# Optimization experiments

Measured on AMD Instinct MI355X. Metric: run time of the kernel, lower is better.

Reference implementation:

```python
import jax, jax.numpy as jnp
import numpy as np

N = 100_000; E = 1_600_000; H = 64
TH = 0.7; ATT_TH = 0.2; EPS = 1e-5

# Heaviside spike with ATan surrogate gradient (spikingjelly default style).
@jax.custom_vjp
def spike_fn(v):
    return (v >= 0.0).astype(v.dtype)

def _spike_fwd(v):
    return spike_fn(v), v

def _spike_bwd(v, g):
    alpha = 2.0
    sg = (alpha / 2.0) / (1.0 + (jnp.pi / 2.0 * alpha * v) ** 2)
    return (g * sg,)

spike_fn.defvjp(_spike_fwd, _spike_bwd)

def lif_step(v, x, th):
    # integrate-and-fire step with hard reset-to-zero
    v = v + x
    s = spike_fn(v - th)
    return s, v * (1.0 - s)

def batchnorm(x, g, b):
    # training-mode BatchNorm1d over the node axis
    m = x.mean(axis=0)
    var = x.var(axis=0)
    return (x - m) * jax.lax.rsqrt(var + EPS) * g + b

def gcn(x, W, b, src, dst, w):
    # PyG GCNConv: xW, add self loops, symmetric deg^-1/2 normalization, scatter-add
    xw = x @ W                                   # [N,H]
    deg = jnp.ones((x.shape[0],), x.dtype).at[dst].add(w)   # self-loop weight 1
    dis = jax.lax.rsqrt(deg)
    norm = dis[src] * w * dis[dst]               # [E]
    agg = jnp.zeros_like(xw).at[dst].add(norm[:, None] * xw[src])
    return agg + (dis * dis)[:, None] * xw + b   # self-loop term + bias

def enc(x, src, dst, w, Wg, bg, bn_g, bn_b, v_conv):
    # Wg order: convs[0], conv, pos_conv, q_lins, k_lins, v_lins, att_conv
    # bn order:  bn_1, bn_2, pos_bn, pos_bn_2, q_bn, k_bn, v_bn, att_bn, att_bn_2
    x = batchnorm(gcn(x, Wg[0], bg[0], src, dst, w), bn_g[0], bn_b[0])
    x, v_conv = lif_step(v_conv, x, TH)          # conv_lif (stateful, never reset)
    x = batchnorm(gcn(x, Wg[1], bg[1], src, dst, w), bn_g[1], bn_b[1])
    z = jnp.zeros_like(x)
    # SGPE positional branch (pos_lif is reset after enc -> fresh state)
    x_pos_spike, _ = lif_step(z, x, TH)
    x_pos = batchnorm(gcn(x_pos_spike, Wg[2], bg[2], src, dst, w), bn_g[2], bn_b[2])
    x = batchnorm(x_pos + x, bn_g[3], bn_b[3])
    # attention branch: conv_lif second (stateful) call
    x_att, v_conv = lif_step(v_conv, x, TH)
    q, _ = lif_step(z, batchnorm(gcn(x_att, Wg[3], bg[3], src, dst, w), bn_g[4], bn_b[4]), TH)
    k, _ = lif_step(z, batchnorm(gcn(x_att, Wg[4], bg[4], src, dst, w), bn_g[5], bn_b[5]), TH)
    v, _ = lif_step(z, batchnorm(gcn(x_att, Wg[5], bg[5], src, dst, w), bn_g[6], bn_b[6]), TH)
    qk = (q * k).mean(axis=1)                    # [N]  (num_attention_heads == 1 path)
    qk, _ = lif_step(jnp.zeros_like(qk), qk, ATT_TH)
    att = qk[:, None] * v                        # repeat(H,1).T * v
    att = batchnorm(gcn(att, Wg[6], bg[6], src, dst, w), bn_g[7], bn_b[7])
    x = batchnorm(x + 0.125 * att, bn_g[8], bn_b[8])
    return x, v_conv

def setup_inputs():
    key = jax.random.key(0)
    ks = jax.random.split(key, 6)
    x = jax.random.normal(ks[0], (N, H), jnp.float32)
    edge_index = jax.random.randint(ks[1], (2, E), 0, N)
    edge_mask = jax.random.randint(ks[2], (E,), 0, 2, jnp.int32)
    Wg = jax.random.normal(ks[3], (7, H, H), jnp.float32) / jnp.sqrt(H)
    bg = jnp.zeros((7, H), jnp.float32)
    bn_g = jnp.ones((9, H), jnp.float32)
    bn_b = jnp.zeros((9, H), jnp.float32)
    W_lin = jax.random.normal(ks[4], (H, H), jnp.float32) / jnp.sqrt(H)
    return {"x": x, "edge_index": edge_index, "edge_mask": edge_mask,
            "Wg": Wg, "bg": bg, "bn_g": bn_g, "bn_b": bn_b, "W_lin": W_lin}

def reference(x, edge_index, edge_mask, Wg, bg, bn_g, bn_b, W_lin):
    src, dst = edge_index[0], edge_index[1]
    w1 = jnp.ones((E,), x.dtype)
    w2 = edge_mask.astype(x.dtype)   # dropout_edge(p=0.2) realized as fixed mask (weight 0 == removed edge)
    v0 = jnp.zeros((N, H), x.dtype)
    s1, v_conv = enc(x, src, dst, w1, Wg, bg, bn_g, bn_b, v0)
    s2, _ = enc(x, src, dst, w2, Wg, bg, bn_g, bn_b, v_conv)  # conv_lif state carries over
    z1 = (s1 @ W_lin).sum(axis=1)    # dec: lin(x).sum(1)
    z2 = (s2 @ W_lin).sum(axis=1)
    return (z1, z2)
```

## Files before the change

### kernel.cpp

```cpp
#include <hip/hip_runtime.h>
#include <math.h>
#include <stdint.h>
#include <limits.h>

#define NN 100000
#define NE 1600000
#define HH 64
#define THF 0.7f
#define ATTTH 0.2f
#define EPSF 1e-5f
#define SCAN_B ((NN + 255) / 256)
#define EM2CAP 1000000
#define NBE 2048
#define NHTOT ((size_t)NN * 64)
#define NB_ROW4C (NN / 4)
#define NTILE (NN / 32)

typedef unsigned long long u64;


__global__ void hist_k(const int* __restrict__ dst, const int* __restrict__ mask,
                       int* __restrict__ cnt_all, int* __restrict__ cnt_mask) {
    int e = blockIdx.x * 256 + threadIdx.x;
    if (e >= NE) return;
    int d = dst[e];
    atomicAdd(&cnt_all[d], 1);
    if (mask[e]) atomicAdd(&cnt_mask[d], 1);
}

__global__ void deg_inv2_k(const int* __restrict__ cnt1, const int* __restrict__ cnt2,
                           float* __restrict__ dis1, float* __restrict__ d21,
                           float* __restrict__ dis2m, float* __restrict__ d22) {
    int i = blockIdx.x * 256 + threadIdx.x;
    if (i < NN) {
        float dg1 = (float)(cnt1[i] + 1);
        dis1[i] = 1.0f / sqrtf(dg1);
        d21[i] = 1.0f / dg1;
        float dg2 = (float)(cnt2[i] + 1);
        dis2m[i] = 1.0f / sqrtf(dg2);
        d22[i] = 1.0f / dg2;
    }
}

__global__ void scan1d_k(const int* __restrict__ cnt1, const int* __restrict__ cnt2,
                         int* __restrict__ rp1, int* __restrict__ rp2,
                         int* __restrict__ bsum) {
    __shared__ int ls[256];
    int half = (blockIdx.x >= SCAN_B) ? 1 : 0;
    int blk = blockIdx.x - half * SCAN_B;
    const int* counts = half ? cnt2 : cnt1;
    int* rp = half ? rp2 : rp1;
    int i = blk * 256 + threadIdx.x;
    int v = (i < NN) ? counts[i] : 0;
    ls[threadIdx.x] = v;
    __syncthreads();
    for (int off = 1; off < 256; off <<= 1) {
        int t = (threadIdx.x >= off) ? ls[threadIdx.x - off] : 0;
        __syncthreads();
        ls[threadIdx.x] += t;
        __syncthreads();
    }
    if (i < NN) rp[i] = ls[threadIdx.x] - v;
    if (threadIdx.x == 255) bsum[blockIdx.x] = ls[255];
}

__global__ __launch_bounds__(512) void scan2d_k(int* __restrict__ bsum,
                                                int* __restrict__ rp1,
                                                int* __restrict__ rp2) {
    __shared__ int ls[512];
    int i = threadIdx.x;
    for (int s = 0; s < 2; s++) {
        int v = (i < SCAN_B) ? bsum[s * SCAN_B + i] : 0;
        ls[i] = v;
        __syncthreads();
        for (int off = 1; off < 512; off <<= 1) {
            int t = (i >= off) ? ls[i - off] : 0;
            __syncthreads();
            ls[i] += t;
            __syncthreads();
        }
        if (i < SCAN_B) bsum[s * SCAN_B + i] = ls[i] - v;
        if (i == SCAN_B - 1) { if (s == 0) rp1[NN] = ls[i]; else rp2[NN] = ls[i]; }
        __syncthreads();
    }
}

__global__ void scan3d_k(int* __restrict__ rp1, int* __restrict__ rp2,
                         const int* __restrict__ bsum) {
    int half = (blockIdx.x >= SCAN_B) ? 1 : 0;
    int blk = blockIdx.x - half * SCAN_B;
    int* rp = half ? rp2 : rp1;
    int i = blk * 256 + threadIdx.x;
    if (i < NN) rp[i] += bsum[blockIdx.x];
}

__global__ void csr_fill_k(const int* __restrict__ src, const int* __restrict__ dst,
                           const int* __restrict__ mask,
                           const int* __restrict__ rp1, const int* __restrict__ rp2,
                           int* __restrict__ cur1, int* __restrict__ cur2,
                           int* __restrict__ emA, int* __restrict__ emB) {
    int e = blockIdx.x * 256 + threadIdx.x;
    if (e >= NE) return;
    int s = src[e], d = dst[e];
    int mk = mask[e] & 1;
    int p1 = rp1[d] + atomicAdd(&cur1[d], 1);
    emA[p1] = (s << 1) | mk;
    if (mk) {
        int p2 = rp2[d] + atomicAdd(&cur2[d], 1);
        emB[p2] = s;
    }
}

__device__ void seg_sort_node(int* __restrict__ em, int beg, int end,
                              int* skey, int lane) {
    int L = end - beg;
    if (L <= 1) return;
    if (L <= 64) {
        int k = (lane < L) ? em[beg + lane] : INT_MAX;
        int rank = 0;
#pragma unroll 8
        for (int r = 0; r < L; r++) {
            int kr = __shfl(k, r, 64);
            rank += (kr < k || (kr == k && r < lane)) ? 1 : 0;
        }
        if (lane < L) em[beg + rank] = k;
    } else if (L <= 512) {
        for (int i = lane; i < L; i += 64) skey[i] = em[beg + i];
        for (int it = 0; it < L; it++) {
            int par = it & 1;
            for (int p = par + 2 * lane; p + 1 < L; p += 128) {
                int ka = skey[p], kb = skey[p + 1];
                if (kb < ka) { skey[p] = kb; skey[p + 1] = ka; }
            }
        }
        for (int i = lane; i < L; i += 64) em[beg + i] = skey[i];
    }
}

__global__ __launch_bounds__(256) void seg_sort2_k(int* __restrict__ emA,
                                                   const int* __restrict__ rp1,
                                                   int* __restrict__ emB,
                                                   const int* __restrict__ rp2) {
    __shared__ int skey[4][512];
    int tid = threadIdx.x, lane = tid & 63, w = tid >> 6;
    int bid = blockIdx.x;
    if (bid < NB_ROW4C) {
        int n = bid * 4 + w;
        seg_sort_node(emA, rp1[n], rp1[n + 1], skey[w], lane);
    } else {
        int n = (bid - NB_ROW4C) * 4 + w;
        seg_sort_node(emB, rp2[n], rp2[n + 1], skey[w], lane);
    }
}


__global__ __launch_bounds__(256) void gemm_k(const float* __restrict__ in,
                                              const float* __restrict__ W,
                                              float* __restrict__ xw) {
    __shared__ float sW[64 * 64];
    __shared__ float sx[32 * 65];
    int tid = threadIdx.x;
    const float4* W4 = (const float4*)W;
    float4* sW4 = (float4*)sW;
    for (int i = tid; i < 1024; i += 256) sW4[i] = W4[i];
    const float* inb = in + (size_t)blockIdx.x * 2048;
    for (int i = tid; i < 2048; i += 256) sx[(i >> 6) * 65 + (i & 63)] = inb[i];
    __syncthreads();
    int cg = tid & 15, rr = tid >> 4;
    float a0 = 0, a1 = 0, a2 = 0, a3 = 0, c0 = 0, c1 = 0, c2 = 0, c3 = 0;
#pragma unroll
    for (int k = 0; k < 64; k++) {
        float4 wv = *(const float4*)&sW[k * 64 + cg * 4];
        float xa = sx[rr * 65 + k];
        float xb = sx[(rr + 16) * 65 + k];
        a0 += xa * wv.x; a1 += xa * wv.y; a2 += xa * wv.z; a3 += xa * wv.w;
        c0 += xb * wv.x; c1 += xb * wv.y; c2 += xb * wv.z; c3 += xb * wv.w;
    }
    size_t r0 = (size_t)(blockIdx.x * 32 + rr) * 64 + cg * 4;
    size_t r1 = (size_t)(blockIdx.x * 32 + rr + 16) * 64 + cg * 4;
    *(float4*)&xw[r0] = make_float4(a0, a1, a2, a3);
    *(float4*)&xw[r1] = make_float4(c0, c1, c2, c3);
}


__global__ __launch_bounds__(256) void gather_stats_k(const float* __restrict__ xw,
                                                      const int* __restrict__ em,
                                                      int shift,
                                                      const float* __restrict__ dis,
                                                      const int* __restrict__ rp,
                                                      const float* __restrict__ d2i,
                                                      const float* __restrict__ bias,
                                                      float* __restrict__ out,
                                                      double* __restrict__ part) {
    int tid = threadIdx.x, lane = tid & 63, w = tid >> 6;
    double ps = 0.0, pq = 0.0;
    for (int n = blockIdx.x * 4 + w; n < NN; n += NBE * 4) {
        int beg = rp[n], end = rp[n + 1];
        float disn = dis[n];
        float self = d2i[n] * xw[(size_t)n * 64 + lane] + bias[lane];
        float acc = 0.0f;
        for (int base = beg; base < end; base += 64) {
            int cnt = min(64, end - base);
            int m = 0; float nl = 0.0f;
            if (base + lane < end) {
                m = em[base + lane];
                nl = dis[m >> shift] * disn;
            }
            int j = 0;
            for (; j + 8 <= cnt; j += 8) {
#pragma unroll
                for (int u = 0; u < 8; u++) {
                    int s = __shfl(m, j + u, 64) >> shift;
                    float nv = __shfl(nl, j + u, 64);
                    acc += nv * xw[(size_t)s * 64 + lane];
                }
            }
            for (; j < cnt; j++) {
                int s = __shfl(m, j, 64) >> shift;
                float nv = __shfl(nl, j, 64);
                acc += nv * xw[(size_t)s * 64 + lane];
            }
        }
        float o = acc + self;
        out[(size_t)n * 64 + lane] = o;
        ps += (double)o;
        pq += (double)o * (double)o;
    }
    __shared__ double ls[4][64], lq[4][64];
    ls[w][lane] = ps; lq[w][lane] = pq;
    __syncthreads();
    if (tid < 64) {
        double a = ls[0][tid] + ls[1][tid] + ls[2][tid] + ls[3][tid];
        double b = lq[0][tid] + lq[1][tid] + lq[2][tid] + lq[3][tid];
        part[(size_t)blockIdx.x * 128 + tid] = a;
        part[(size_t)blockIdx.x * 128 + 64 + tid] = b;
    }
}

__global__ __launch_bounds__(256) void sharedL0_k(const float* __restrict__ xw,
                                                  const int* __restrict__ em,
                                                  const int* __restrict__ rp,
                                                  const float* __restrict__ dis1,
                                                  const float* __restrict__ dis2m,
                                                  const float* __restrict__ d21,
                                                  const float* __restrict__ d22,
                                                  const float* __restrict__ bias,
                                                  float* __restrict__ o1,
                                                  float* __restrict__ o2,
                                                  double* __restrict__ part) {
    int tid = threadIdx.x, lane = tid & 63, w = tid >> 6;
    double sA = 0.0, qA = 0.0, sB = 0.0, qB = 0.0;
    for (int n = blockIdx.x * 4 + w; n < NN; n += NBE * 4) {
        int beg = rp[n], end = rp[n + 1];
        float disn1 = dis1[n], disn2 = dis2m[n];
        float xv = xw[(size_t)n * 64 + lane];
        float self1 = d21[n] * xv + bias[lane];
        float self2 = d22[n] * xv + bias[lane];
        float acc1 = 0.0f, acc2 = 0.0f;
        for (int base = beg; base < end; base += 64) {
            int cnt = min(64, end - base);
            int m = 0; float nl1 = 0.0f, nl2 = 0.0f;
            if (base + lane < end) {
                m = em[base + lane];
                int s = m >> 1;
                nl1 = dis1[s] * disn1;
                nl2 = dis2m[s] * disn2;
            }
            int j = 0;
            for (; j + 8 <= cnt; j += 8) {
#pragma unroll
                for (int u = 0; u < 8; u++) {
                    int key = __shfl(m, j + u, 64);
                    int s = key >> 1;
                    float n1 = __shfl(nl1, j + u, 64);
                    float n2 = __shfl(nl2, j + u, 64);
                    float v = xw[(size_t)s * 64 + lane];
                    acc1 += n1 * v;
                    acc2 += (key & 1) ? n2 * v : 0.0f;
                }
            }
            for (; j < cnt; j++) {
                int key = __shfl(m, j, 64);
                int s = key >> 1;
                float n1 = __shfl(nl1, j, 64);
                float n2 = __shfl(nl2, j, 64);
                float v = xw[(size_t)s * 64 + lane];
                acc1 += n1 * v;
                acc2 += (key & 1) ? n2 * v : 0.0f;
            }
        }
        size_t o = (size_t)n * 64 + lane;
        float v1 = acc1 + self1;
        float v2 = acc2 + self2;
        o1[o] = v1;
        o2[o] = v2;
        sA += (double)v1; qA += (double)v1 * (double)v1;
        sB += (double)v2; qB += (double)v2 * (double)v2;
    }
    __shared__ double l1[4][64], l2[4][64], l3[4][64], l4[4][64];
    l1[w][lane] = sA; l2[w][lane] = qA; l3[w][lane] = sB; l4[w][lane] = qB;
    __syncthreads();
    if (tid < 64) {
        size_t o = (size_t)blockIdx.x * 256;
        part[o + tid]       = l1[0][tid] + l1[1][tid] + l1[2][tid] + l1[3][tid];
        part[o + 64 + tid]  = l2[0][tid] + l2[1][tid] + l2[2][tid] + l2[3][tid];
        part[o + 128 + tid] = l3[0][tid] + l3[1][tid] + l3[2][tid] + l3[3][tid];
        part[o + 192 + tid] = l4[0][tid] + l4[1][tid] + l4[2][tid] + l4[3][tid];
    }
}


__global__ __launch_bounds__(256) void bitagg_k(const u64* __restrict__ bits,
                                                const int* __restrict__ em,
                                                int shift,
                                                const float* __restrict__ dis,
                                                const int* __restrict__ rp,
                                                const float* __restrict__ d2i,
                                                float* __restrict__ A) {
    int tid = threadIdx.x, lane = tid & 63, w = tid >> 6;
    int sh31 = lane & 31;
    bool islo = lane < 32;
    for (int n = blockIdx.x * 4 + w; n < NN; n += NBE * 4) {
        int beg = rp[n], end = rp[n + 1];
        float disn = dis[n];
        float acc = 0.0f;
        for (int base = beg; base < end; base += 64) {
            int cnt = min(64, end - base);
            unsigned blo = 0, bhi = 0; float nl = 0.0f;
            if (base + lane < end) {
                int m = em[base + lane];
                int s = m >> shift;
                nl = dis[s] * disn;
                u64 b = bits[s];
                blo = (unsigned)b;
                bhi = (unsigned)(b >> 32);
            }
            int j = 0;
            for (; j + 8 <= cnt; j += 8) {
#pragma unroll
                for (int u = 0; u < 8; u++) {
                    float nv = __shfl(nl, j + u, 64);
                    unsigned lo = (unsigned)__shfl((int)blo, j + u, 64);
                    unsigned hi = (unsigned)__shfl((int)bhi, j + u, 64);
                    unsigned sel = islo ? lo : hi;
                    acc += ((sel >> sh31) & 1u) ? nv : 0.0f;
                }
            }
            for (; j < cnt; j++) {
                float nv = __shfl(nl, j, 64);
                unsigned lo = (unsigned)__shfl((int)blo, j, 64);
                unsigned hi = (unsigned)__shfl((int)bhi, j, 64);
                unsigned sel = islo ? lo : hi;
                acc += ((sel >> sh31) & 1u) ? nv : 0.0f;
            }
        }
        u64 bn = bits[n];
        unsigned seln = islo ? (unsigned)bn : (unsigned)(bn >> 32);
        acc += ((seln >> sh31) & 1u) ? d2i[n] : 0.0f;
        A[(size_t)n * 64 + lane] = acc;
    }
}


__global__ __launch_bounds__(256) void gemmb_stats_k(const float* __restrict__ A,
                                                     const float* __restrict__ W,
                                                     const float* __restrict__ bias,
                                                     float* __restrict__ G,
                                                     double* __restrict__ part,
                                                     int pstride, int pbase) {
    __shared__ float sW[64 * 64];
    __shared__ float sx[32 * 65];
    __shared__ double sS[64][16], sQ[64][16];
    int tid = threadIdx.x;
    const float4* W4 = (const float4*)W;
    float4* sW4 = (float4*)sW;
    for (int i = tid; i < 1024; i += 256) sW4[i] = W4[i];
    int cg = tid & 15, rr = tid >> 4;
    float4 bv = *(const float4*)&bias[cg * 4];
    double s0 = 0, s1 = 0, s2 = 0, s3 = 0, q0 = 0, q1 = 0, q2 = 0, q3 = 0;
    for (int tile = blockIdx.x; tile < NTILE; tile += NBE) {
        const float* Ab = A + (size_t)tile * 2048;
        __syncthreads();
        for (int i = tid; i < 2048; i += 256) sx[(i >> 6) * 65 + (i & 63)] = Ab[i];
        __syncthreads();
        float a0 = bv.x, a1 = bv.y, a2 = bv.z, a3 = bv.w;
        float c0 = bv.x, c1 = bv.y, c2 = bv.z, c3 = bv.w;
#pragma unroll
        for (int k = 0; k < 64; k++) {
            float4 wv = *(const float4*)&sW[k * 64 + cg * 4];
            float xa = sx[rr * 65 + k];
            float xb = sx[(rr + 16) * 65 + k];
            a0 += xa * wv.x; a1 += xa * wv.y; a2 += xa * wv.z; a3 += xa * wv.w;
            c0 += xb * wv.x; c1 += xb * wv.y; c2 += xb * wv.z; c3 += xb * wv.w;
        }
        size_t r0 = (size_t)(tile * 32 + rr) * 64 + cg * 4;
        size_t r1 = (size_t)(tile * 32 + rr + 16) * 64 + cg * 4;
        *(float4*)&G[r0] = make_float4(a0, a1, a2, a3);
        *(float4*)&G[r1] = make_float4(c0, c1, c2, c3);
        s0 += (double)a0; s0 += (double)c0;
        s1 += (double)a1; s1 += (double)c1;
        s2 += (double)a2; s2 += (double)c2;
        s3 += (double)a3; s3 += (double)c3;
        q0 += (double)a0 * (double)a0; q0 += (double)c0 * (double)c0;
        q1 += (double)a1 * (double)a1; q1 += (double)c1 * (double)c1;
        q2 += (double)a2 * (double)a2; q2 += (double)c2 * (double)c2;
        q3 += (double)a3 * (double)a3; q3 += (double)c3 * (double)c3;
    }
    __syncthreads();
    sS[cg * 4 + 0][rr] = s0; sQ[cg * 4 + 0][rr] = q0;
    sS[cg * 4 + 1][rr] = s1; sQ[cg * 4 + 1][rr] = q1;
    sS[cg * 4 + 2][rr] = s2; sQ[cg * 4 + 2][rr] = q2;
    sS[cg * 4 + 3][rr] = s3; sQ[cg * 4 + 3][rr] = q3;
    __syncthreads();
    if (tid < 64) {
        double a = 0.0, b = 0.0;
#pragma unroll
        for (int r = 0; r < 16; r++) { a += sS[tid][r]; b += sQ[tid][r]; }
        part[(size_t)blockIdx.x * pstride + pbase + tid] = a;
        part[(size_t)blockIdx.x * pstride + pbase + 64 + tid] = b;
    }
}


__global__ __launch_bounds__(256) void bn_red_k(const double* __restrict__ part,
                                                double* __restrict__ st) {
    __shared__ double tr[256];
    int t = threadIdx.x, c = blockIdx.x;
    double s = 0.0;
    for (int b = t; b < NBE; b += 256) s += part[(size_t)b * 128 + c];
    tr[t] = s;
    __syncthreads();
    for (int off = 128; off > 0; off >>= 1) {
        if (t < off) tr[t] += tr[t + off];
        __syncthreads();
    }
    if (t == 0) st[c] = tr[0];
}

__global__ __launch_bounds__(256) void bn_red2_k(const double* __restrict__ part,
                                                 double* __restrict__ sta,
                                                 double* __restrict__ stb) {
    __shared__ double tr[256];
    int t = threadIdx.x, c = blockIdx.x;
    double s = 0.0;
    for (int b = t; b < NBE; b += 256) s += part[(size_t)b * 256 + c];
    tr[t] = s;
    __syncthreads();
    for (int off = 128; off > 0; off >>= 1) {
        if (t < off) tr[t] += tr[t + off];
        __syncthreads();
    }
    if (t == 0) {
        if (c < 128) sta[c] = tr[0];
        else stb[c - 128] = tr[0];
    }
}

__global__ __launch_bounds__(256) void bn_red3_k(const double* __restrict__ part,
                                                 double* __restrict__ sta,
                                                 double* __restrict__ stb,
                                                 double* __restrict__ stc) {
    __shared__ double tr[256];
    int t = threadIdx.x, c = blockIdx.x;
    double s = 0.0;
    for (int b = t; b < NBE; b += 256) s += part[(size_t)b * 384 + c];
    tr[t] = s;
    __syncthreads();
    for (int off = 128; off > 0; off >>= 1) {
        if (t < off) tr[t] += tr[t + off];
        __syncthreads();
    }
    if (t == 0) {
        if (c < 128) sta[c] = tr[0];
        else if (c < 256) stb[c - 128] = tr[0];
        else stc[c - 256] = tr[0];
    }
}

__device__ inline void bn_ss(const double* __restrict__ st, const float* __restrict__ gam,
                             const float* __restrict__ bet, int c,
                             float* __restrict__ ssc, float* __restrict__ ssh) {
    double m = st[c] * (1.0 / NN);
    double v = st[64 + c] * (1.0 / NN) - m * m;
    float scale = (float)((double)gam[c] / sqrt(v + (double)EPSF));
    ssc[c] = scale;
    ssh[c] = bet[c] - (float)m * scale;
}


__global__ __launch_bounds__(256) void lif_spike_k(const float* __restrict__ G,
                                                   const double* __restrict__ st,
                                                   const float* __restrict__ gam,
                                                   const float* __restrict__ bet,
                                                   float* __restrict__ vconv,
                                                   u64* __restrict__ bits) {
    __shared__ float ssc[64], ssh[64];
    int tid = threadIdx.x;
    if (tid < 64) bn_ss(st, gam, bet, tid, ssc, ssh);
    __syncthreads();
    int lane = tid & 63;
    size_t i = (size_t)blockIdx.x * 256 + tid;
    float v = vconv[i] + (G[i] * ssc[lane] + ssh[lane]);
    bool sp = (v - THF >= 0.0f);
    u64 m = __ballot(sp);
    vconv[i] = sp ? 0.0f : v;
    if (lane == 0) bits[i >> 6] = m;
}

__global__ __launch_bounds__(256) void spike_save_k(const float* __restrict__ G,
                                                    const double* __restrict__ st,
                                                    const float* __restrict__ gam,
                                                    const float* __restrict__ bet,
                                                    float* __restrict__ xsave,
                                                    u64* __restrict__ bits) {
    __shared__ float ssc[64], ssh[64];
    int tid = threadIdx.x;
    if (tid < 64) bn_ss(st, gam, bet, tid, ssc, ssh);
    __syncthreads();
    int lane = tid & 63;
    size_t i = (size_t)blockIdx.x * 256 + tid;
    float xv = G[i] * ssc[lane] + ssh[lane];
    xsave[i] = xv;
    u64 m = __ballot(xv - THF >= 0.0f);
    if (lane == 0) bits[i >> 6] = m;
}

__global__ __launch_bounds__(256) void lif_spike_save_k(const float* __restrict__ F,
                                                        const double* __restrict__ st,
                                                        const float* __restrict__ gam,
                                                        const float* __restrict__ bet,
                                                        float* __restrict__ vconv,
                                                        float* __restrict__ xsave,
                                                        u64* __restrict__ bits) {
    __shared__ float ssc[64], ssh[64];
    int tid = threadIdx.x;
    if (tid < 64) bn_ss(st, gam, bet, tid, ssc, ssh);
    __syncthreads();
    int lane = tid & 63;
    size_t i = (size_t)blockIdx.x * 256 + tid;
    float xv = F[i] * ssc[lane] + ssh[lane];
    xsave[i] = xv;
    float v = vconv[i] + xv;
    bool sp = (v - THF >= 0.0f);
    u64 m = __ballot(sp);
    vconv[i] = sp ? 0.0f : v;
    if (lane == 0) bits[i >> 6] = m;
}

__global__ __launch_bounds__(256) void qkv_att_spike_k(const float* __restrict__ Gq,
                                                       const float* __restrict__ Gk,
                                                       const float* __restrict__ Gv,
                                                       const double* __restrict__ st4,
                                                       const double* __restrict__ st5,
                                                       const double* __restrict__ st6,
                                                       const float* __restrict__ gam4,
                                                       const float* __restrict__ bet4,
                                                       const float* __restrict__ gam5,
                                                       const float* __restrict__ bet5,
                                                       const float* __restrict__ gam6,
                                                       const float* __restrict__ bet6,
                                                       u64* __restrict__ bits) {
    __shared__ float sc4[64], sh4[64], sc5[64], sh5[64], sc6[64], sh6[64];
    int tid = threadIdx.x;
    if (tid < 64) {
        bn_ss(st4, gam4, bet4, tid, sc4, sh4);
        bn_ss(st5, gam5, bet5, tid, sc5, sh5);
        bn_ss(st6, gam6, bet6, tid, sc6, sh6);
    }
    __syncthreads();
    int lane = tid & 63;
    size_t i = (size_t)blockIdx.x * 256 + tid;
    bool qb = (Gq[i] * sc4[lane] + sh4[lane] - THF >= 0.0f);
    bool kb = (Gk[i] * sc5[lane] + sh5[lane] - THF >= 0.0f);
    bool vb = (Gv[i] * sc6[lane] + sh6[lane] - THF >= 0.0f);
    int pc = __popcll(__ballot(qb && kb));
    bool qs = ((float)pc * (1.0f / 64.0f) - ATTTH >= 0.0f);
    u64 m = __ballot(vb && qs);
    if (lane == 0) bits[i >> 6] = m;
}


__global__ __launch_bounds__(256) void bn_add_stats_k(const float* __restrict__ G,
                                                      const double* __restrict__ st,
                                                      const float* __restrict__ gam,
                                                      const float* __restrict__ bet,
                                                      const float* __restrict__ x3,
                                                      float* __restrict__ F,
                                                      double* __restrict__ part) {
    __shared__ float ssc[64], ssh[64];
    int tid = threadIdx.x;
    if (tid < 64) bn_ss(st, gam, bet, tid, ssc, ssh);
    __syncthreads();
    int c = tid & 63;
    double s = 0.0, s2 = 0.0;
    for (size_t i = (size_t)blockIdx.x * 256 + tid; i < NHTOT; i += (size_t)NBE * 256) {
        float f = (G[i] * ssc[c] + ssh[c]) + x3[i];
        F[i] = f;
        s += (double)f;
        s2 += (double)f * (double)f;
    }
    __shared__ double ls[256], lq[256];
    ls[tid] = s; lq[tid] = s2;
    __syncthreads();
    if (tid < 64) {
        double a = ls[tid] + ls[tid + 64] + ls[tid + 128] + ls[tid + 192];
        double b = lq[tid] + lq[tid + 64] + lq[tid + 128] + lq[tid + 192];
        part[(size_t)blockIdx.x * 128 + tid] = a;
        part[(size_t)blockIdx.x * 128 + 64 + tid] = b;
    }
}

__global__ __launch_bounds__(256) void bn_scale_add_stats_k(const float* __restrict__ G,
                                                            const double* __restrict__ st,
                                                            const float* __restrict__ gam,
                                                            const float* __restrict__ bet,
                                                            const float* __restrict__ x4,
                                                            float* __restrict__ tmp2,
                                                            double* __restrict__ part) {
    __shared__ float ssc[64], ssh[64];
    int tid = threadIdx.x;
    if (tid < 64) bn_ss(st, gam, bet, tid, ssc, ssh);
    __syncthreads();
    int c = tid & 63;
    double s = 0.0, s2 = 0.0;
    for (size_t i = (size_t)blockIdx.x * 256 + tid; i < NHTOT; i += (size_t)NBE * 256) {
        float f = x4[i] + 0.125f * (G[i] * ssc[c] + ssh[c]);
        tmp2[i] = f;
        s += (double)f;
        s2 += (double)f * (double)f;
    }
    __shared__ double ls[256], lq[256];
    ls[tid] = s; lq[tid] = s2;
    __syncthreads();
    if (tid < 64) {
        double a = ls[tid] + ls[tid + 64] + ls[tid + 128] + ls[tid + 192];
        double b = lq[tid] + lq[tid + 64] + lq[tid + 128] + lq[tid + 192];
        part[(size_t)blockIdx.x * 128 + tid] = a;
        part[(size_t)blockIdx.x * 128 + 64 + tid] = b;
    }
}

__global__ __launch_bounds__(256) void decode_k(const float* __restrict__ tmp2,
                                                const double* __restrict__ st,
                                                const float* __restrict__ gam,
                                                const float* __restrict__ bet,
                                                const float* __restrict__ wrow,
                                                float* __restrict__ z) {
    __shared__ float ssc[64], ssh[64];
    int tid = threadIdx.x;
    if (tid < 64) bn_ss(st, gam, bet, tid, ssc, ssh);
    __syncthreads();
    int lane = tid & 63;
    int row = blockIdx.x * 4 + (tid >> 6);
    float sv = tmp2[(size_t)row * 64 + lane] * ssc[lane] + ssh[lane];
    float p = sv * wrow[lane];
#pragma unroll
    for (int off = 32; off > 0; off >>= 1) p += __shfl_xor(p, off, 64);
    if (lane == 0) z[row] = p;
}

__global__ void wrow_k(const float* __restrict__ W_lin, float* __restrict__ wrow) {
    int h = threadIdx.x;
    if (h >= 64) return;
    float s = 0.0f;
    for (int j = 0; j < 64; j++) s += W_lin[h * 64 + j];
    wrow[h] = s;
}


extern "C" void kernel_launch(void* const* d_in, const int* in_sizes, int n_in,
                              void* d_out, int out_size, void* d_ws, size_t ws_size,
                              hipStream_t stream) {
    const float* x    = (const float*)d_in[0];
    const int* eidx   = (const int*)d_in[1];
    const int* emask  = (const int*)d_in[2];
    const float* Wg   = (const float*)d_in[3];
    const float* bg   = (const float*)d_in[4];
    const float* bng  = (const float*)d_in[5];
    const float* bnb  = (const float*)d_in[6];
    const float* Wlin = (const float*)d_in[7];
    float* zout = (float*)d_out;

    const int* srcp = eidx;
    const int* dstp = eidx + NE;
    const size_t NH = (size_t)NN * HH;

    float* ws = (float*)d_ws;
    size_t off = 0;
    float* P1 = ws + off; off += NH;
    float* P2 = ws + off; off += NH;
    float* P3 = ws + off; off += NH;
    float* P4 = ws + off; off += NH;
    float* P5 = ws + off; off += NH;
    float* vconv = ws + off; off += NH;
    int* emA = (int*)(ws + off); off += NE;
    int* emB = (int*)(ws + off); off += EM2CAP;
    u64* sbits = (u64*)(ws + off); off += 2 * (size_t)NN;
    double* part = (double*)(ws + off); off += 2 * (size_t)NBE * 384;
    double* stats = (double*)(ws + off); off += 2 * 18 * 128;
    float* dis1 = ws + off; off += NN;
    float* d21  = ws + off; off += NN;
    float* dis2m = ws + off; off += NN;
    float* d22  = ws + off; off += NN;
    float* wrow = ws + off; off += 64;
    int* rp1 = (int*)(ws + off); off += NN + 2;
    int* rp2 = (int*)(ws + off); off += NN + 2;
    int* cnt1 = (int*)(ws + off); off += NN;
    int* cnt2 = (int*)(ws + off); off += NN;
    int* cur1 = (int*)(ws + off); off += NN;
    int* cur2 = (int*)(ws + off); off += NN + 2;
    int* bsum = (int*)(ws + off); off += 2 * SCAN_B + 4;
    if (off & 1) off++;
    float* P8 = ws + off; off += NH;
    size_t needA2 = off * 4;
    const bool tA2 = (ws_size >= needA2);

    hipMemsetAsync(cnt1, 0, 4 * NN * sizeof(int), stream);
    hipMemsetAsync(vconv, 0, NH * sizeof(float), stream);

    const int NB_EDGE = NE / 256;
    const int NB_ROW4 = NN / 4;
    const int NB_GEMM = NN / 32;

    wrow_k<<<1, 64, 0, stream>>>(Wlin, wrow);
    hist_k<<<NB_EDGE, 256, 0, stream>>>(dstp, emask, cnt1, cnt2);
    deg_inv2_k<<<SCAN_B, 256, 0, stream>>>(cnt1, cnt2, dis1, d21, dis2m, d22);
    scan1d_k<<<2 * SCAN_B, 256, 0, stream>>>(cnt1, cnt2, rp1, rp2, bsum);
    scan2d_k<<<1, 512, 0, stream>>>(bsum, rp1, rp2);
    scan3d_k<<<2 * SCAN_B, 256, 0, stream>>>(rp1, rp2, bsum);
    csr_fill_k<<<NB_EDGE, 256, 0, stream>>>(srcp, dstp, emask, rp1, rp2,
                                            cur1, cur2, emA, emB);
    seg_sort2_k<<<2 * NB_ROW4C, 256, 0, stream>>>(emA, rp1, emB, rp2);

    auto enc = [&](const int* em, int shift, const float* dis, const int* rp,
                   const float* d2i, int bnbase, float* zo, const float* G0pre) {
        auto ST = [&](int bni) { return stats + (bnbase + bni) * 128; };
        auto W = [&](int wi) { return Wg + wi * 4096; };
        auto BI = [&](int wi) { return bg + wi * 64; };
        auto GM = [&](int bi) { return bng + bi * 64; };
        auto BT = [&](int bi) { return bnb + bi * 64; };

        const float* G0 = G0pre;
        if (!G0) {
            gemm_k<<<NB_GEMM, 256, 0, stream>>>(x, W(0), P1);
            gather_stats_k<<<NBE, 256, 0, stream>>>(P1, em, shift, dis, rp, d2i,
                                                    BI(0), P2, part);
            bn_red_k<<<128, 256, 0, stream>>>(part, ST(0));
            G0 = P2;
        }
        lif_spike_k<<<NB_ROW4, 256, 0, stream>>>(G0, ST(0), GM(0), BT(0), vconv, sbits);
        bitagg_k<<<NBE, 256, 0, stream>>>(sbits, em, shift, dis, rp, d2i, P1);
        gemmb_stats_k<<<NBE, 256, 0, stream>>>(P1, W(1), BI(1), P5, part, 128, 0);
        bn_red_k<<<128, 256, 0, stream>>>(part, ST(1));
        spike_save_k<<<NB_ROW4, 256, 0, stream>>>(P5, ST(1), GM(1), BT(1), P3, sbits);
        bitagg_k<<<NBE, 256, 0, stream>>>(sbits, em, shift, dis, rp, d2i, P1);
        gemmb_stats_k<<<NBE, 256, 0, stream>>>(P1, W(2), BI(2), P5, part, 128, 0);
        bn_red_k<<<128, 256, 0, stream>>>(part, ST(2));
        bn_add_stats_k<<<NBE, 256, 0, stream>>>(P5, ST(2), GM(2), BT(2), P3, P4, part);
        bn_red_k<<<128, 256, 0, stream>>>(part, ST(3));
        lif_spike_save_k<<<NB_ROW4, 256, 0, stream>>>(P4, ST(3), GM(3), BT(3),
                                                      vconv, P4, sbits);
        bitagg_k<<<NBE, 256, 0, stream>>>(sbits, em, shift, dis, rp, d2i, P1);
        gemmb_stats_k<<<NBE, 256, 0, stream>>>(P1, W(3), BI(3), P2, part, 384, 0);
        gemmb_stats_k<<<NBE, 256, 0, stream>>>(P1, W(4), BI(4), P3, part, 384, 128);
        gemmb_stats_k<<<NBE, 256, 0, stream>>>(P1, W(5), BI(5), P5, part, 384, 256);
        bn_red3_k<<<384, 256, 0, stream>>>(part, ST(4), ST(5), ST(6));
        qkv_att_spike_k<<<NB_ROW4, 256, 0, stream>>>(P2, P3, P5,
                                                     ST(4), ST(5), ST(6),
                                                     GM(4), BT(4), GM(5), BT(5),
                                                     GM(6), BT(6), sbits);
        bitagg_k<<<NBE, 256, 0, stream>>>(sbits, em, shift, dis, rp, d2i, P1);
        gemmb_stats_k<<<NBE, 256, 0, stream>>>(P1, W(6), BI(6), P2, part, 128, 0);
        bn_red_k<<<128, 256, 0, stream>>>(part, ST(7));
        bn_scale_add_stats_k<<<NBE, 256, 0, stream>>>(P2, ST(7), GM(7), BT(7),
                                                      P4, P3, part);
        bn_red_k<<<128, 256, 0, stream>>>(part, ST(8));
        decode_k<<<NB_ROW4, 256, 0, stream>>>(P3, ST(8), GM(8), BT(8), wrow, zo);
    };

    if (tA2) {
        gemm_k<<<NB_GEMM, 256, 0, stream>>>(x, Wg, P1);
        sharedL0_k<<<NBE, 256, 0, stream>>>(P1, emA, rp1, dis1, dis2m, d21, d22,
                                            bg, P2, P8, part);
        bn_red2_k<<<256, 256, 0, stream>>>(part, stats + 0 * 128, stats + 9 * 128);
        enc(emA, 1, dis1, rp1, d21, 0, zout, P2);
        enc(emB, 0, dis2m, rp2, d22, 9, zout + NN, P8);
    } else {
        enc(emA, 1, dis1, rp1, d21, 0, zout, nullptr);
        enc(emB, 0, dis2m, rp2, d22, 9, zout + NN, nullptr);
    }
}
```

Before: 1.570 ms.

## Replace partial-sum reduction kernels with double atomics and reuse hist ranks

Batch-norm statistics are now accumulated directly into the stats buffer with double-precision atomic adds from each block, which removes the separate bn_red/bn_red2/bn_red3 launches and the large partials buffer. The histogram kernel records each edge's rank within its destination and the CSR fill reuses it, so the second round of atomics and the cursor arrays go away. The degree-inverse computation is folded into the scan kernel, removing one more launch. In exchange there is contention from 2048 blocks on 128 atomics per stat and summation order becomes nondeterministic. Rank packing into 16 bits assumes in-degree stays below 65536.

```diff
diff --git a/kernel.cpp b/kernel.cpp
--- a/kernel.cpp
+++ b/kernel.cpp
@@ -20,31 +20,22 @@
 
 
 __global__ void hist_k(const int* __restrict__ dst, const int* __restrict__ mask,
-                       int* __restrict__ cnt_all, int* __restrict__ cnt_mask) {
+                       int* __restrict__ cnt_all, int* __restrict__ cnt_mask,
+                       int* __restrict__ rk) {
     int e = blockIdx.x * 256 + threadIdx.x;
     if (e >= NE) return;
     int d = dst[e];
-    atomicAdd(&cnt_all[d], 1);
-    if (mask[e]) atomicAdd(&cnt_mask[d], 1);
-}
-
-__global__ void deg_inv2_k(const int* __restrict__ cnt1, const int* __restrict__ cnt2,
-                           float* __restrict__ dis1, float* __restrict__ d21,
-                           float* __restrict__ dis2m, float* __restrict__ d22) {
-    int i = blockIdx.x * 256 + threadIdx.x;
-    if (i < NN) {
-        float dg1 = (float)(cnt1[i] + 1);
-        dis1[i] = 1.0f / sqrtf(dg1);
-        d21[i] = 1.0f / dg1;
-        float dg2 = (float)(cnt2[i] + 1);
-        dis2m[i] = 1.0f / sqrtf(dg2);
-        d22[i] = 1.0f / dg2;
-    }
+    int r1 = atomicAdd(&cnt_all[d], 1);
+    int r2 = 0;
+    if (mask[e]) r2 = atomicAdd(&cnt_mask[d], 1);
+    rk[e] = r1 | (r2 << 16);
 }
 
 __global__ void scan1d_k(const int* __restrict__ cnt1, const int* __restrict__ cnt2,
                          int* __restrict__ rp1, int* __restrict__ rp2,
-                         int* __restrict__ bsum) {
+                         int* __restrict__ bsum,
+                         float* __restrict__ dis1, float* __restrict__ d21,
+                         float* __restrict__ dis2m, float* __restrict__ d22) {
     __shared__ int ls[256];
     int half = (blockIdx.x >= SCAN_B) ? 1 : 0;
     int blk = blockIdx.x - half * SCAN_B;
@@ -52,6 +43,13 @@
     int* rp = half ? rp2 : rp1;
     int i = blk * 256 + threadIdx.x;
     int v = (i < NN) ? counts[i] : 0;
+    if (i < NN) {
+        float dg = (float)(v + 1);
+        float is = 1.0f / sqrtf(dg);
+        float iv = 1.0f / dg;
+        if (half) { dis2m[i] = is; d22[i] = iv; }
+        else      { dis1[i] = is;  d21[i] = iv; }
+    }
     ls[threadIdx.x] = v;
     __syncthreads();
     for (int off = 1; off < 256; off <<= 1) {
@@ -95,20 +93,16 @@
 }
 
 __global__ void csr_fill_k(const int* __restrict__ src, const int* __restrict__ dst,
-                           const int* __restrict__ mask,
+                           const int* __restrict__ mask, const int* __restrict__ rk,
                            const int* __restrict__ rp1, const int* __restrict__ rp2,
-                           int* __restrict__ cur1, int* __restrict__ cur2,
                            int* __restrict__ emA, int* __restrict__ emB) {
     int e = blockIdx.x * 256 + threadIdx.x;
     if (e >= NE) return;
     int s = src[e], d = dst[e];
     int mk = mask[e] & 1;
-    int p1 = rp1[d] + atomicAdd(&cur1[d], 1);
-    emA[p1] = (s << 1) | mk;
-    if (mk) {
-        int p2 = rp2[d] + atomicAdd(&cur2[d], 1);
-        emB[p2] = s;
-    }
+    int r = rk[e];
+    emA[rp1[d] + (r & 0xFFFF)] = (s << 1) | mk;
+    if (mk) emB[rp2[d] + (r >> 16)] = s;
 }
 
 __device__ void seg_sort_node(int* __restrict__ em, int beg, int end,
@@ -191,7 +185,7 @@
                                                       const float* __restrict__ d2i,
                                                       const float* __restrict__ bias,
                                                       float* __restrict__ out,
-                                                      double* __restrict__ part) {
+                                                      double* __restrict__ st) {
     int tid = threadIdx.x, lane = tid & 63, w = tid >> 6;
     double ps = 0.0, pq = 0.0;
     for (int n = blockIdx.x * 4 + w; n < NN; n += NBE * 4) {
@@ -232,8 +226,8 @@
     if (tid < 64) {
         double a = ls[0][tid] + ls[1][tid] + ls[2][tid] + ls[3][tid];
         double b = lq[0][tid] + lq[1][tid] + lq[2][tid] + lq[3][tid];
-        part[(size_t)blockIdx.x * 128 + tid] = a;
-        part[(size_t)blockIdx.x * 128 + 64 + tid] = b;
+        unsafeAtomicAdd(&st[tid], a);
+        unsafeAtomicAdd(&st[64 + tid], b);
     }
 }
 
@@ -247,7 +241,8 @@
                                                   const float* __restrict__ bias,
                                                   float* __restrict__ o1,
                                                   float* __restrict__ o2,
-                                                  double* __restrict__ part) {
+                                                  double* __restrict__ st1,
+                                                  double* __restrict__ st2) {
     int tid = threadIdx.x, lane = tid & 63, w = tid >> 6;
     double sA = 0.0, qA = 0.0, sB = 0.0, qB = 0.0;
     for (int n = blockIdx.x * 4 + w; n < NN; n += NBE * 4) {
@@ -301,11 +296,10 @@
     l1[w][lane] = sA; l2[w][lane] = qA; l3[w][lane] = sB; l4[w][lane] = qB;
     __syncthreads();
     if (tid < 64) {
-        size_t o = (size_t)blockIdx.x * 256;
-        part[o + tid]       = l1[0][tid] + l1[1][tid] + l1[2][tid] + l1[3][tid];
-        part[o + 64 + tid]  = l2[0][tid] + l2[1][tid] + l2[2][tid] + l2[3][tid];
-        part[o + 128 + tid] = l3[0][tid] + l3[1][tid] + l3[2][tid] + l3[3][tid];
-        part[o + 192 + tid] = l4[0][tid] + l4[1][tid] + l4[2][tid] + l4[3][tid];
+        unsafeAtomicAdd(&st1[tid],      l1[0][tid] + l1[1][tid] + l1[2][tid] + l1[3][tid]);
+        unsafeAtomicAdd(&st1[64 + tid], l2[0][tid] + l2[1][tid] + l2[2][tid] + l2[3][tid]);
+        unsafeAtomicAdd(&st2[tid],      l3[0][tid] + l3[1][tid] + l3[2][tid] + l3[3][tid]);
+        unsafeAtomicAdd(&st2[64 + tid], l4[0][tid] + l4[1][tid] + l4[2][tid] + l4[3][tid]);
     }
 }
 
@@ -366,11 +360,10 @@
                                                      const float* __restrict__ W,
                                                      const float* __restrict__ bias,
                                                      float* __restrict__ G,
-                                                     double* __restrict__ part,
-                                                     int pstride, int pbase) {
-    __shared__ float sW[64 * 64];
-    __shared__ float sx[32 * 65];
-    __shared__ double sS[64][16], sQ[64][16];
+                                                     double* __restrict__ st) {
+    __shared__ float smem[4096 + 2112];
+    float* sW = smem;
+    float* sx = smem + 4096;
     int tid = threadIdx.x;
     const float4* W4 = (const float4*)W;
     float4* sW4 = (float4*)sW;
@@ -407,75 +400,22 @@
         q3 += (double)a3 * (double)a3; q3 += (double)c3 * (double)c3;
     }
     __syncthreads();
-    sS[cg * 4 + 0][rr] = s0; sQ[cg * 4 + 0][rr] = q0;
-    sS[cg * 4 + 1][rr] = s1; sQ[cg * 4 + 1][rr] = q1;
-    sS[cg * 4 + 2][rr] = s2; sQ[cg * 4 + 2][rr] = q2;
-    sS[cg * 4 + 3][rr] = s3; sQ[cg * 4 + 3][rr] = q3;
+    double* sS = (double*)smem;
+    double* sQ = sS + 64 * 17;
+    sS[(cg * 4 + 0) * 17 + rr] = s0; sQ[(cg * 4 + 0) * 17 + rr] = q0;
+    sS[(cg * 4 + 1) * 17 + rr] = s1; sQ[(cg * 4 + 1) * 17 + rr] = q1;
+    sS[(cg * 4 + 2) * 17 + rr] = s2; sQ[(cg * 4 + 2) * 17 + rr] = q2;
+    sS[(cg * 4 + 3) * 17 + rr] = s3; sQ[(cg * 4 + 3) * 17 + rr] = q3;
     __syncthreads();
     if (tid < 64) {
         double a = 0.0, b = 0.0;
 #pragma unroll
-        for (int r = 0; r < 16; r++) { a += sS[tid][r]; b += sQ[tid][r]; }
-        part[(size_t)blockIdx.x * pstride + pbase + tid] = a;
-        part[(size_t)blockIdx.x * pstride + pbase + 64 + tid] = b;
-    }
-}
-
-
-__global__ __launch_bounds__(256) void bn_red_k(const double* __restrict__ part,
-                                                double* __restrict__ st) {
-    __shared__ double tr[256];
-    int t = threadIdx.x, c = blockIdx.x;
-    double s = 0.0;
-    for (int b = t; b < NBE; b += 256) s += part[(size_t)b * 128 + c];
-    tr[t] = s;
-    __syncthreads();
-    for (int off = 128; off > 0; off >>= 1) {
-        if (t < off) tr[t] += tr[t + off];
-        __syncthreads();
-    }
-    if (t == 0) st[c] = tr[0];
-}
-
-__global__ __launch_bounds__(256) void bn_red2_k(const double* __restrict__ part,
-                                                 double* __restrict__ sta,
-                                                 double* __restrict__ stb) {
-    __shared__ double tr[256];
-    int t = threadIdx.x, c = blockIdx.x;
-    double s = 0.0;
-    for (int b = t; b < NBE; b += 256) s += part[(size_t)b * 256 + c];
-    tr[t] = s;
-    __syncthreads();
-    for (int off = 128; off > 0; off >>= 1) {
-        if (t < off) tr[t] += tr[t + off];
-        __syncthreads();
-    }
-    if (t == 0) {
-        if (c < 128) sta[c] = tr[0];
-        else stb[c - 128] = tr[0];
-    }
-}
-
-__global__ __launch_bounds__(256) void bn_red3_k(const double* __restrict__ part,
-                                                 double* __restrict__ sta,
-                                                 double* __restrict__ stb,
-                                                 double* __restrict__ stc) {
-    __shared__ double tr[256];
-    int t = threadIdx.x, c = blockIdx.x;
-    double s = 0.0;
-    for (int b = t; b < NBE; b += 256) s += part[(size_t)b * 384 + c];
-    tr[t] = s;
-    __syncthreads();
-    for (int off = 128; off > 0; off >>= 1) {
-        if (t < off) tr[t] += tr[t + off];
-        __syncthreads();
-    }
-    if (t == 0) {
-        if (c < 128) sta[c] = tr[0];
-        else if (c < 256) stb[c - 128] = tr[0];
-        else stc[c - 256] = tr[0];
-    }
-}
+        for (int r = 0; r < 16; r++) { a += sS[tid * 17 + r]; b += sQ[tid * 17 + r]; }
+        unsafeAtomicAdd(&st[tid], a);
+        unsafeAtomicAdd(&st[64 + tid], b);
+    }
+}
+
 
 __device__ inline void bn_ss(const double* __restrict__ st, const float* __restrict__ gam,
                              const float* __restrict__ bet, int c,
@@ -586,7 +526,7 @@
                                                       const float* __restrict__ bet,
                                                       const float* __restrict__ x3,
                                                       float* __restrict__ F,
-                                                      double* __restrict__ part) {
+                                                      double* __restrict__ sto) {
     __shared__ float ssc[64], ssh[64];
     int tid = threadIdx.x;
     if (tid < 64) bn_ss(st, gam, bet, tid, ssc, ssh);
@@ -605,8 +545,8 @@
     if (tid < 64) {
         double a = ls[tid] + ls[tid + 64] + ls[tid + 128] + ls[tid + 192];
         double b = lq[tid] + lq[tid + 64] + lq[tid + 128] + lq[tid + 192];
-        part[(size_t)blockIdx.x * 128 + tid] = a;
-        part[(size_t)blockIdx.x * 128 + 64 + tid] = b;
+        unsafeAtomicAdd(&sto[tid], a);
+        unsafeAtomicAdd(&sto[64 + tid], b);
     }
 }
 
@@ -616,7 +556,7 @@
                                                             const float* __restrict__ bet,
                                                             const float* __restrict__ x4,
                                                             float* __restrict__ tmp2,
-                                                            double* __restrict__ part) {
+                                                            double* __restrict__ sto) {
     __shared__ float ssc[64], ssh[64];
     int tid = threadIdx.x;
     if (tid < 64) bn_ss(st, gam, bet, tid, ssc, ssh);
@@ -635,8 +575,8 @@
     if (tid < 64) {
         double a = ls[tid] + ls[tid + 64] + ls[tid + 128] + ls[tid + 192];
         double b = lq[tid] + lq[tid + 64] + lq[tid + 128] + lq[tid + 192];
-        part[(size_t)blockIdx.x * 128 + tid] = a;
-        part[(size_t)blockIdx.x * 128 + 64 + tid] = b;
+        unsafeAtomicAdd(&sto[tid], a);
+        unsafeAtomicAdd(&sto[64 + tid], b);
     }
 }
 
@@ -696,8 +636,8 @@
     int* emA = (int*)(ws + off); off += NE;
     int* emB = (int*)(ws + off); off += EM2CAP;
     u64* sbits = (u64*)(ws + off); off += 2 * (size_t)NN;
-    double* part = (double*)(ws + off); off += 2 * (size_t)NBE * 384;
     double* stats = (double*)(ws + off); off += 2 * 18 * 128;
+    int* rk = (int*)(ws + off); off += NE;
     float* dis1 = ws + off; off += NN;
     float* d21  = ws + off; off += NN;
     float* dis2m = ws + off; off += NN;
@@ -707,15 +647,14 @@
     int* rp2 = (int*)(ws + off); off += NN + 2;
     int* cnt1 = (int*)(ws + off); off += NN;
     int* cnt2 = (int*)(ws + off); off += NN;
-    int* cur1 = (int*)(ws + off); off += NN;
-    int* cur2 = (int*)(ws + off); off += NN + 2;
     int* bsum = (int*)(ws + off); off += 2 * SCAN_B + 4;
     if (off & 1) off++;
     float* P8 = ws + off; off += NH;
     size_t needA2 = off * 4;
     const bool tA2 = (ws_size >= needA2);
 
-    hipMemsetAsync(cnt1, 0, 4 * NN * sizeof(int), stream);
+    hipMemsetAsync(cnt1, 0, 2 * NN * sizeof(int), stream);
+    hipMemsetAsync(stats, 0, 18 * 128 * sizeof(double), stream);
     hipMemsetAsync(vconv, 0, NH * sizeof(float), stream);
 
     const int NB_EDGE = NE / 256;
@@ -723,13 +662,13 @@
     const int NB_GEMM = NN / 32;
 
     wrow_k<<<1, 64, 0, stream>>>(Wlin, wrow);
-    hist_k<<<NB_EDGE, 256, 0, stream>>>(dstp, emask, cnt1, cnt2);
-    deg_inv2_k<<<SCAN_B, 256, 0, stream>>>(cnt1, cnt2, dis1, d21, dis2m, d22);
-    scan1d_k<<<2 * SCAN_B, 256, 0, stream>>>(cnt1, cnt2, rp1, rp2, bsum);
+    hist_k<<<NB_EDGE, 256, 0, stream>>>(dstp, emask, cnt1, cnt2, rk);
+    scan1d_k<<<2 * SCAN_B, 256, 0, stream>>>(cnt1, cnt2, rp1, rp2, bsum,
+                                             dis1, d21, dis2m, d22);
     scan2d_k<<<1, 512, 0, stream>>>(bsum, rp1, rp2);
     scan3d_k<<<2 * SCAN_B, 256, 0, stream>>>(rp1, rp2, bsum);
-    csr_fill_k<<<NB_EDGE, 256, 0, stream>>>(srcp, dstp, emask, rp1, rp2,
-                                            cur1, cur2, emA, emB);
+    csr_fill_k<<<NB_EDGE, 256, 0, stream>>>(srcp, dstp, emask, rk, rp1, rp2,
+                                            emA, emB);
     seg_sort2_k<<<2 * NB_ROW4C, 256, 0, stream>>>(emA, rp1, emB, rp2);
 
     auto enc = [&](const int* em, int shift, const float* dis, const int* rp,
@@ -744,45 +683,38 @@
         if (!G0) {
             gemm_k<<<NB_GEMM, 256, 0, stream>>>(x, W(0), P1);
             gather_stats_k<<<NBE, 256, 0, stream>>>(P1, em, shift, dis, rp, d2i,
-                                                    BI(0), P2, part);
-            bn_red_k<<<128, 256, 0, stream>>>(part, ST(0));
+                                                    BI(0), P2, ST(0));
             G0 = P2;
         }
         lif_spike_k<<<NB_ROW4, 256, 0, stream>>>(G0, ST(0), GM(0), BT(0), vconv, sbits);
         bitagg_k<<<NBE, 256, 0, stream>>>(sbits, em, shift, dis, rp, d2i, P1);
-        gemmb_stats_k<<<NBE, 256, 0, stream>>>(P1, W(1), BI(1), P5, part, 128, 0);
-        bn_red_k<<<128, 256, 0, stream>>>(part, ST(1));
+        gemmb_stats_k<<<NBE, 256, 0, stream>>>(P1, W(1), BI(1), P5, ST(1));
         spike_save_k<<<NB_ROW4, 256, 0, stream>>>(P5, ST(1), GM(1), BT(1), P3, sbits);
         bitagg_k<<<NBE, 256, 0, stream>>>(sbits, em, shift, dis, rp, d2i, P1);
-        gemmb_stats_k<<<NBE, 256, 0, stream>>>(P1, W(2), BI(2), P5, part, 128, 0);
-        bn_red_k<<<128, 256, 0, stream>>>(part, ST(2));
-        bn_add_stats_k<<<NBE, 256, 0, stream>>>(P5, ST(2), GM(2), BT(2), P3, P4, part);
-        bn_red_k<<<128, 256, 0, stream>>>(part, ST(3));
+        gemmb_stats_k<<<NBE, 256, 0, stream>>>(P1, W(2), BI(2), P5, ST(2));
+        bn_add_stats_k<<<NBE, 256, 0, stream>>>(P5, ST(2), GM(2), BT(2), P3, P4, ST(3));
         lif_spike_save_k<<<NB_ROW4, 256, 0, stream>>>(P4, ST(3), GM(3), BT(3),
                                                       vconv, P4, sbits);
         bitagg_k<<<NBE, 256, 0, stream>>>(sbits, em, shift, dis, rp, d2i, P1);
-        gemmb_stats_k<<<NBE, 256, 0, stream>>>(P1, W(3), BI(3), P2, part, 384, 0);
-        gemmb_stats_k<<<NBE, 256, 0, stream>>>(P1, W(4), BI(4), P3, part, 384, 128);
-        gemmb_stats_k<<<NBE, 256, 0, stream>>>(P1, W(5), BI(5), P5, part, 384, 256);
-        bn_red3_k<<<384, 256, 0, stream>>>(part, ST(4), ST(5), ST(6));
+        gemmb_stats_k<<<NBE, 256, 0, stream>>>(P1, W(3), BI(3), P2, ST(4));
+        gemmb_stats_k<<<NBE, 256, 0, stream>>>(P1, W(4), BI(4), P3, ST(5));
+        gemmb_stats_k<<<NBE, 256, 0, stream>>>(P1, W(5), BI(5), P5, ST(6));
         qkv_att_spike_k<<<NB_ROW4, 256, 0, stream>>>(P2, P3, P5,
                                                      ST(4), ST(5), ST(6),
                                                      GM(4), BT(4), GM(5), BT(5),
                                                      GM(6), BT(6), sbits);
         bitagg_k<<<NBE, 256, 0, stream>>>(sbits, em, shift, dis, rp, d2i, P1);
-        gemmb_stats_k<<<NBE, 256, 0, stream>>>(P1, W(6), BI(6), P2, part, 128, 0);
-        bn_red_k<<<128, 256, 0, stream>>>(part, ST(7));
+        gemmb_stats_k<<<NBE, 256, 0, stream>>>(P1, W(6), BI(6), P2, ST(7));
         bn_scale_add_stats_k<<<NBE, 256, 0, stream>>>(P2, ST(7), GM(7), BT(7),
-                                                      P4, P3, part);
-        bn_red_k<<<128, 256, 0, stream>>>(part, ST(8));
+                                                      P4, P3, ST(8));
         decode_k<<<NB_ROW4, 256, 0, stream>>>(P3, ST(8), GM(8), BT(8), wrow, zo);
     };
 
     if (tA2) {
         gemm_k<<<NB_GEMM, 256, 0, stream>>>(x, Wg, P1);
         sharedL0_k<<<NBE, 256, 0, stream>>>(P1, emA, rp1, dis1, dis2m, d21, d22,
-                                            bg, P2, P8, part);
-        bn_red2_k<<<256, 256, 0, stream>>>(part, stats + 0 * 128, stats + 9 * 128);
+                                            bg, P2, P8,
+                                            stats + 0 * 128, stats + 9 * 128);
         enc(emA, 1, dis1, rp1, d21, 0, zout, P2);
         enc(emB, 0, dis2m, rp2, d22, 9, zout + NN, P8);
     } else {
```

Result: slower. 1.908 ms (+21.5%).

## Record per-edge ranks in histogram pass to drop CSR fill atomics

Applied to the files above, without the earlier changes.

The histogram kernel now stores each edge's atomic return value (its rank within the destination bucket) in a new per-edge array, so the CSR fill kernel computes write positions directly instead of issuing a second round of atomics on cursor arrays. The degree-inverse kernel is folded into the first scan kernel, removing one launch, and the cursor memset shrinks. The GEMM-stats kernel reuses one shared buffer for its tile data and reduction scratch with padded rows, cutting LDS footprint and bank conflicts. The cost is an extra 6.4MB of per-edge rank traffic, and packing two ranks into 16 bits each assumes no node has 65536 or more incoming edges.

```diff
diff --git a/kernel.cpp b/kernel.cpp
--- a/kernel.cpp
+++ b/kernel.cpp
@@ -20,31 +20,22 @@
 
 
 __global__ void hist_k(const int* __restrict__ dst, const int* __restrict__ mask,
-                       int* __restrict__ cnt_all, int* __restrict__ cnt_mask) {
+                       int* __restrict__ cnt_all, int* __restrict__ cnt_mask,
+                       int* __restrict__ rk) {
     int e = blockIdx.x * 256 + threadIdx.x;
     if (e >= NE) return;
     int d = dst[e];
-    atomicAdd(&cnt_all[d], 1);
-    if (mask[e]) atomicAdd(&cnt_mask[d], 1);
-}
-
-__global__ void deg_inv2_k(const int* __restrict__ cnt1, const int* __restrict__ cnt2,
-                           float* __restrict__ dis1, float* __restrict__ d21,
-                           float* __restrict__ dis2m, float* __restrict__ d22) {
-    int i = blockIdx.x * 256 + threadIdx.x;
-    if (i < NN) {
-        float dg1 = (float)(cnt1[i] + 1);
-        dis1[i] = 1.0f / sqrtf(dg1);
-        d21[i] = 1.0f / dg1;
-        float dg2 = (float)(cnt2[i] + 1);
-        dis2m[i] = 1.0f / sqrtf(dg2);
-        d22[i] = 1.0f / dg2;
-    }
+    int r1 = atomicAdd(&cnt_all[d], 1);
+    int r2 = 0;
+    if (mask[e]) r2 = atomicAdd(&cnt_mask[d], 1);
+    rk[e] = r1 | (r2 << 16);
 }
 
 __global__ void scan1d_k(const int* __restrict__ cnt1, const int* __restrict__ cnt2,
                          int* __restrict__ rp1, int* __restrict__ rp2,
-                         int* __restrict__ bsum) {
+                         int* __restrict__ bsum,
+                         float* __restrict__ dis1, float* __restrict__ d21,
+                         float* __restrict__ dis2m, float* __restrict__ d22) {
     __shared__ int ls[256];
     int half = (blockIdx.x >= SCAN_B) ? 1 : 0;
     int blk = blockIdx.x - half * SCAN_B;
@@ -52,6 +43,13 @@
     int* rp = half ? rp2 : rp1;
     int i = blk * 256 + threadIdx.x;
     int v = (i < NN) ? counts[i] : 0;
+    if (i < NN) {
+        float dg = (float)(v + 1);
+        float is = 1.0f / sqrtf(dg);
+        float iv = 1.0f / dg;
+        if (half) { dis2m[i] = is; d22[i] = iv; }
+        else      { dis1[i] = is;  d21[i] = iv; }
+    }
     ls[threadIdx.x] = v;
     __syncthreads();
     for (int off = 1; off < 256; off <<= 1) {
@@ -95,20 +93,16 @@
 }
 
 __global__ void csr_fill_k(const int* __restrict__ src, const int* __restrict__ dst,
-                           const int* __restrict__ mask,
+                           const int* __restrict__ mask, const int* __restrict__ rk,
                            const int* __restrict__ rp1, const int* __restrict__ rp2,
-                           int* __restrict__ cur1, int* __restrict__ cur2,
                            int* __restrict__ emA, int* __restrict__ emB) {
     int e = blockIdx.x * 256 + threadIdx.x;
     if (e >= NE) return;
     int s = src[e], d = dst[e];
     int mk = mask[e] & 1;
-    int p1 = rp1[d] + atomicAdd(&cur1[d], 1);
-    emA[p1] = (s << 1) | mk;
-    if (mk) {
-        int p2 = rp2[d] + atomicAdd(&cur2[d], 1);
-        emB[p2] = s;
-    }
+    int r = rk[e];
+    emA[rp1[d] + (r & 0xFFFF)] = (s << 1) | mk;
+    if (mk) emB[rp2[d] + (r >> 16)] = s;
 }
 
 __device__ void seg_sort_node(int* __restrict__ em, int beg, int end,
@@ -368,9 +362,9 @@
                                                      float* __restrict__ G,
                                                      double* __restrict__ part,
                                                      int pstride, int pbase) {
-    __shared__ float sW[64 * 64];
-    __shared__ float sx[32 * 65];
-    __shared__ double sS[64][16], sQ[64][16];
+    __shared__ float smem[4096 + 2112];
+    float* sW = smem;
+    float* sx = smem + 4096;
     int tid = threadIdx.x;
     const float4* W4 = (const float4*)W;
     float4* sW4 = (float4*)sW;
@@ -407,15 +401,17 @@
         q3 += (double)a3 * (double)a3; q3 += (double)c3 * (double)c3;
     }
     __syncthreads();
-    sS[cg * 4 + 0][rr] = s0; sQ[cg * 4 + 0][rr] = q0;
-    sS[cg * 4 + 1][rr] = s1; sQ[cg * 4 + 1][rr] = q1;
-    sS[cg * 4 + 2][rr] = s2; sQ[cg * 4 + 2][rr] = q2;
-    sS[cg * 4 + 3][rr] = s3; sQ[cg * 4 + 3][rr] = q3;
+    double* sS = (double*)smem;
+    double* sQ = sS + 64 * 17;
+    sS[(cg * 4 + 0) * 17 + rr] = s0; sQ[(cg * 4 + 0) * 17 + rr] = q0;
+    sS[(cg * 4 + 1) * 17 + rr] = s1; sQ[(cg * 4 + 1) * 17 + rr] = q1;
+    sS[(cg * 4 + 2) * 17 + rr] = s2; sQ[(cg * 4 + 2) * 17 + rr] = q2;
+    sS[(cg * 4 + 3) * 17 + rr] = s3; sQ[(cg * 4 + 3) * 17 + rr] = q3;
     __syncthreads();
     if (tid < 64) {
         double a = 0.0, b = 0.0;
 #pragma unroll
-        for (int r = 0; r < 16; r++) { a += sS[tid][r]; b += sQ[tid][r]; }
+        for (int r = 0; r < 16; r++) { a += sS[tid * 17 + r]; b += sQ[tid * 17 + r]; }
         part[(size_t)blockIdx.x * pstride + pbase + tid] = a;
         part[(size_t)blockIdx.x * pstride + pbase + 64 + tid] = b;
     }
@@ -698,6 +694,7 @@
     u64* sbits = (u64*)(ws + off); off += 2 * (size_t)NN;
     double* part = (double*)(ws + off); off += 2 * (size_t)NBE * 384;
     double* stats = (double*)(ws + off); off += 2 * 18 * 128;
+    int* rk = (int*)(ws + off); off += NE;
     float* dis1 = ws + off; off += NN;
     float* d21  = ws + off; off += NN;
     float* dis2m = ws + off; off += NN;
@@ -707,15 +704,13 @@
     int* rp2 = (int*)(ws + off); off += NN + 2;
     int* cnt1 = (int*)(ws + off); off += NN;
     int* cnt2 = (int*)(ws + off); off += NN;
-    int* cur1 = (int*)(ws + off); off += NN;
-    int* cur2 = (int*)(ws + off); off += NN + 2;
     int* bsum = (int*)(ws + off); off += 2 * SCAN_B + 4;
     if (off & 1) off++;
     float* P8 = ws + off; off += NH;
     size_t needA2 = off * 4;
     const bool tA2 = (ws_size >= needA2);
 
-    hipMemsetAsync(cnt1, 0, 4 * NN * sizeof(int), stream);
+    hipMemsetAsync(cnt1, 0, 2 * NN * sizeof(int), stream);
     hipMemsetAsync(vconv, 0, NH * sizeof(float), stream);
 
     const int NB_EDGE = NE / 256;
@@ -723,13 +718,13 @@
     const int NB_GEMM = NN / 32;
 
     wrow_k<<<1, 64, 0, stream>>>(Wlin, wrow);
-    hist_k<<<NB_EDGE, 256, 0, stream>>>(dstp, emask, cnt1, cnt2);
-    deg_inv2_k<<<SCAN_B, 256, 0, stream>>>(cnt1, cnt2, dis1, d21, dis2m, d22);
-    scan1d_k<<<2 * SCAN_B, 256, 0, stream>>>(cnt1, cnt2, rp1, rp2, bsum);
+    hist_k<<<NB_EDGE, 256, 0, stream>>>(dstp, emask, cnt1, cnt2, rk);
+    scan1d_k<<<2 * SCAN_B, 256, 0, stream>>>(cnt1, cnt2, rp1, rp2, bsum,
+                                             dis1, d21, dis2m, d22);
     scan2d_k<<<1, 512, 0, stream>>>(bsum, rp1, rp2);
     scan3d_k<<<2 * SCAN_B, 256, 0, stream>>>(rp1, rp2, bsum);
-    csr_fill_k<<<NB_EDGE, 256, 0, stream>>>(srcp, dstp, emask, rp1, rp2,
-                                            cur1, cur2, emA, emB);
+    csr_fill_k<<<NB_EDGE, 256, 0, stream>>>(srcp, dstp, emask, rk, rp1, rp2,
+                                            emA, emB);
     seg_sort2_k<<<2 * NB_ROW4C, 256, 0, stream>>>(emA, rp1, emB, rp2);
 
     auto enc = [&](const int* em, int shift, const float* dis, const int* rp,
```

Measured after the change: 1.452 ms. 7.5% less time.
